# Optimization experiments

Hardware: AMD Instinct MI355X
Metric: run time of the kernel (lower is better)

The kernel has to match this reference:

```python
import jax, jax.numpy as jnp
import numpy as np
from jax import lax

CURRICULUM_EP = 12
LI, LS, LW = 0.5, 0.8, 3.0


def _gauss_win(ws, C, dtype):
    coords = jnp.arange(ws, dtype=jnp.float32) - ws // 2
    g = jnp.exp(-coords ** 2 / (2 * 1.5 ** 2))
    win = g[None, :] * g[:, None]
    win = win / win.sum()
    # depthwise kernel, OIHW with I=1, O=C
    return jnp.broadcast_to(win[None, None], (C, 1, ws, ws)).astype(dtype)


def _dwconv(x, win, p, C):
    return lax.conv_general_dilated(
        x, win, window_strides=(1, 1), padding=[(p, p), (p, p)],
        dimension_numbers=('NCHW', 'OIHW', 'NCHW'), feature_group_count=C)


def diff_ssim(x, y, ws=11):
    C1, C2 = 0.01 ** 2, 0.03 ** 2
    C = x.shape[1]
    p = ws // 2
    win = _gauss_win(ws, C, x.dtype)
    mx = _dwconv(x, win, p, C)
    my = _dwconv(y, win, p, C)
    sxx = _dwconv(x * x, win, p, C) - mx ** 2
    syy = _dwconv(y * y, win, p, C) - my ** 2
    sxy = _dwconv(x * y, win, p, C) - mx * my
    ssim_map = (2 * mx * my + C1) * (2 * sxy + C2) / ((mx ** 2 + my ** 2 + C1) * (sxx + syy + C2))
    return ssim_map.mean()


def setup_inputs() -> dict:
    key = jax.random.key(0)
    k1, k2, k3, k4 = jax.random.split(key, 4)
    B, C, H, W = 16, 3, 512, 512
    NB = 1024  # watermark bits
    eps = 1e-4
    cover = jax.random.uniform(k1, (B, C, H, W), dtype=jnp.float32)
    wmed = jax.random.uniform(k2, (B, C, H, W), dtype=jnp.float32)
    wm_orig = jax.random.uniform(k3, (B, NB), dtype=jnp.float32)
    wm_ext = jnp.clip(jax.random.uniform(k4, (B, NB), dtype=jnp.float32), eps, 1.0 - eps)
    return {"cover": cover, "wmed": wmed, "wm_orig": wm_orig, "wm_ext": wm_ext, "epoch": 20}


def reference(cover, wmed, wm_orig, wm_ext, epoch):
    ml = jnp.mean((wmed - cover) ** 2)
    sv = diff_ssim(wmed, cover)
    sl = 1.0 - sv
    wl = jnp.mean(-(wm_orig * jnp.log(wm_ext) + (1.0 - wm_orig) * jnp.log(1.0 - wm_ext)))
    if epoch <= CURRICULUM_EP:
        w_img, w_ssim = 0.05, 0.05
    else:
        progress = min(1.0, (epoch - CURRICULUM_EP) / 10.0)
        w_img = 0.05 + (LI - 0.05) * progress
        w_ssim = 0.05 + (LS - 0.05) * progress
    total = w_img * ml + w_ssim * sl + LW * wl
    return (total, ml, sv, wl)
```

## Files before the change

### kernel.cpp

```cpp
#include <hip/hip_runtime.h>
#include <math.h>

#define H_IMG 512
#define W_IMG 512
#define TW 32
#define CH 32
#define NCHUNK 4
#define STRIP (CH*NCHUNK)
#define HALO 5
#define WS11 11
#define RING 42
#define RS 36
#define FSTR (RING*RS)
#define NTHREADS 256

typedef float f2 __attribute__((ext_vector_type(2)));

__host__ __device__ constexpr float WT(int t) {
    return (t==0||t==10) ? 0.00102838f :
           (t==1||t==9)  ? 0.00759873f :
           (t==2||t==8)  ? 0.03600075f :
           (t==3||t==7)  ? 0.10936070f :
           (t==4||t==6)  ? 0.21300556f :
           (t==5)        ? 0.26601172f : 0.0f;
}

static __device__ __forceinline__ f2 splat2(float v) { f2 r = {v, v}; return r; }

__global__ __launch_bounds__(NTHREADS, 5) void ssim_mse_tile(
        const float* __restrict__ cover, const float* __restrict__ wmed,
        float* __restrict__ part, int nParts) {
    __shared__ __align__(16) float rbuf[5*FSTR];

    const int tid = threadIdx.x;
    const int bx  = blockIdx.x & 15;
    const int ys  = (blockIdx.x >> 4) & 3;
    const int pl  = blockIdx.x >> 6;
    const size_t pbase = (size_t)pl * (H_IMG*W_IMG);
    const float* xp = wmed + pbase;
    const float* yp = cover + pbase;
    const int Y0  = ys << 7;
    const int tx0 = bx*TW - HALO;
    const bool xin = (bx != 0) && (bx != 15);

    float ssim_acc = 0.f, mse_acc = 0.f;

    for (int k = 0; k < NCHUNK; ++k) {
        const int nrows = (k == 0) ? (CH + 2*HALO) : CH;
        const int hr0   = (k == 0) ? -HALO : (CH*k + HALO);
        const int ntask = nrows << 3;

        for (int t = tid; t < ntask; t += NTHREADS) {
            const int r  = t >> 3, c0 = (t & 7) << 2;
            const int hr = hr0 + r;
            const int gy = Y0 + hr;
            const int slot = (hr + HALO) % RING;
            const bool rok = (unsigned)gy < (unsigned)H_IMG;
            float xv[14], yv[14];
            if (rok && xin) {
                const int ga = tx0 + c0 - 3;
                const float* rx = xp + (size_t)gy*W_IMG + ga;
                const float* ry = yp + (size_t)gy*W_IMG + ga;
                float4 XA = *(const float4*)(rx);
                float4 XB = *(const float4*)(rx + 4);
                float4 XC = *(const float4*)(rx + 8);
                float4 XD = *(const float4*)(rx + 12);
                float  XE = rx[16];
                float4 YA = *(const float4*)(ry);
                float4 YB = *(const float4*)(ry + 4);
                float4 YC = *(const float4*)(ry + 8);
                float4 YD = *(const float4*)(ry + 12);
                float  YE = ry[16];
                xv[0]=XA.w;  xv[1]=XB.x;  xv[2]=XB.y;  xv[3]=XB.z;  xv[4]=XB.w;
                xv[5]=XC.x;  xv[6]=XC.y;  xv[7]=XC.z;  xv[8]=XC.w;  xv[9]=XD.x;
                xv[10]=XD.y; xv[11]=XD.z; xv[12]=XD.w; xv[13]=XE;
                yv[0]=YA.w;  yv[1]=YB.x;  yv[2]=YB.y;  yv[3]=YB.z;  yv[4]=YB.w;
                yv[5]=YC.x;  yv[6]=YC.y;  yv[7]=YC.z;  yv[8]=YC.w;  yv[9]=YD.x;
                yv[10]=YD.y; yv[11]=YD.z; yv[12]=YD.w; yv[13]=YE;
            } else if (rok) {
                const int gc = tx0 + c0;
                const float* prx = xp + (size_t)gy*W_IMG + gc;
                const float* pry = yp + (size_t)gy*W_IMG + gc;
#pragma unroll
                for (int j = 0; j < 14; ++j) {
                    bool ok = (unsigned)(gc + j) < (unsigned)W_IMG;
                    xv[j] = ok ? prx[j] : 0.f;
                    yv[j] = ok ? pry[j] : 0.f;
                }
            } else {
#pragma unroll
                for (int j = 0; j < 14; ++j) { xv[j] = 0.f; yv[j] = 0.f; }
            }

            if ((unsigned)hr < (unsigned)STRIP) {
#pragma unroll
                for (int j = 5; j < 9; ++j) {
                    float d = xv[j] - yv[j];
                    mse_acc = fmaf(d, d, mse_acc);
                }
            }

            f2 A[5][2];
#pragma unroll
            for (int f = 0; f < 5; ++f) { A[f][0] = splat2(0.f); A[f][1] = splat2(0.f); }
#pragma unroll
            for (int j = 0; j < 14; ++j) {
                float px = xv[j], py = yv[j];
                float pxx = px*px, pyy = py*py, pxy = px*py;
#pragma unroll
                for (int p = 0; p < 2; ++p) {
                    const int t0 = j - 2*p;
                    if (t0 >= 0 && t0 <= WS11) {
                        const f2 wp = {WT(t0), WT(t0-1)};
                        A[0][p] = __builtin_elementwise_fma(wp, splat2(px),  A[0][p]);
                        A[1][p] = __builtin_elementwise_fma(wp, splat2(py),  A[1][p]);
                        A[2][p] = __builtin_elementwise_fma(wp, splat2(pxx), A[2][p]);
                        A[3][p] = __builtin_elementwise_fma(wp, splat2(pyy), A[3][p]);
                        A[4][p] = __builtin_elementwise_fma(wp, splat2(pxy), A[4][p]);
                    }
                }
            }
            float* wb = &rbuf[slot*RS + c0];
#pragma unroll
            for (int f = 0; f < 5; ++f) {
                *(float4*)(wb + f*FSTR) =
                    make_float4(A[f][0].x, A[f][0].y, A[f][1].x, A[f][1].y);
            }
        }
        __syncthreads();

        {
            const int c  = tid & 31;
            const int rg = tid >> 3 >> 2;
            const int sb = (CH*k + (rg << 2)) % RING;
            f2 acc[5][2];
#pragma unroll
            for (int f = 0; f < 5; ++f) {
                acc[f][0] = splat2(0.f); acc[f][1] = splat2(0.f);
            }
            const float* bp = rbuf + c;
#pragma unroll
            for (int i = 0; i < 14; ++i) {
                int sl = sb + i; if (sl >= RING) sl -= RING;
                const float* rp = bp + sl*RS;
#pragma unroll
                for (int f = 0; f < 5; ++f) {
                    float v = rp[f*FSTR];
#pragma unroll
                    for (int p = 0; p < 2; ++p) {
                        const int t0 = i - 2*p;
                        if (t0 >= 0 && t0 <= WS11) {
                            const f2 wp = {WT(t0), WT(t0-1)};
                            acc[f][p] = __builtin_elementwise_fma(wp, splat2(v), acc[f][p]);
                        }
                    }
                }
            }
            const f2 c1v = {1e-4f, 1e-4f};
            const f2 c2v = {9e-4f, 9e-4f};
            const f2 two = {2.f, 2.f};
#pragma unroll
            for (int p = 0; p < 2; ++p) {
                f2 mx = acc[0][p], my = acc[1][p];
                f2 sxx = acc[2][p] - mx*mx;
                f2 syy = acc[3][p] - my*my;
                f2 sxy = acc[4][p] - mx*my;
                f2 num = (two*mx*my + c1v) * (two*sxy + c2v);
                f2 den = (mx*mx + my*my + c1v) * (sxx + syy + c2v);
                ssim_acc += __fdividef(num.x, den.x) + __fdividef(num.y, den.y);
            }
        }
        __syncthreads();
    }

#pragma unroll
    for (int off = 32; off > 0; off >>= 1) {
        ssim_acc += __shfl_down(ssim_acc, off);
        mse_acc  += __shfl_down(mse_acc, off);
    }
    const int wid = tid >> 6, lane = tid & 63;
    if (lane == 0) { rbuf[wid] = ssim_acc; rbuf[4+wid] = mse_acc; }
    __syncthreads();
    if (tid == 0) {
        part[blockIdx.x] = rbuf[0]+rbuf[1]+rbuf[2]+rbuf[3];
        part[nParts + blockIdx.x] = rbuf[4]+rbuf[5]+rbuf[6]+rbuf[7];
    }
}

#define FT 1024
__global__ __launch_bounds__(FT) void finalize_k(
        const float* __restrict__ part, int nParts,
        const float* __restrict__ wm_orig, const float* __restrict__ wm_ext,
        int nWm, const int* __restrict__ epoch_p,
        float* __restrict__ out, double inv_npix, double inv_nwm) {
    __shared__ double red[48];
    int tid = threadIdx.x;
    double s_ssim = 0.0, s_mse = 0.0, s_wl = 0.0;
    const float4* s4 = (const float4*)part;
    const float4* m4 = (const float4*)(part + nParts);
    int n4 = nParts >> 2;
    for (int i = tid; i < n4; i += FT) {
        float4 v = s4[i];
        s_ssim += (double)((v.x + v.y) + (v.z + v.w));
        float4 u = m4[i];
        s_mse  += (double)((u.x + u.y) + (u.z + u.w));
    }
    const float4* p4 = (const float4*)wm_orig;
    const float4* q4 = (const float4*)wm_ext;
    int w4 = nWm >> 2;
    for (int i = tid; i < w4; i += FT) {
        float4 p = p4[i], q = q4[i];
        float a;
        a  = -(p.x*__logf(q.x) + (1.f-p.x)*__logf(1.f-q.x));
        a += -(p.y*__logf(q.y) + (1.f-p.y)*__logf(1.f-q.y));
        a += -(p.z*__logf(q.z) + (1.f-p.z)*__logf(1.f-q.z));
        a += -(p.w*__logf(q.w) + (1.f-p.w)*__logf(1.f-q.w));
        s_wl += (double)a;
    }
#pragma unroll
    for (int off = 32; off > 0; off >>= 1) {
        s_ssim += __shfl_down(s_ssim, off);
        s_mse  += __shfl_down(s_mse, off);
        s_wl   += __shfl_down(s_wl, off);
    }
    int wid = tid >> 6, lane = tid & 63;
    if (lane == 0) { red[wid] = s_ssim; red[16+wid] = s_mse; red[32+wid] = s_wl; }
    __syncthreads();
    if (tid == 0) {
        double ssim_sum = 0.0, mse_sum = 0.0, wl_sum = 0.0;
        for (int i = 0; i < 16; ++i) {
            ssim_sum += red[i]; mse_sum += red[16+i]; wl_sum += red[32+i];
        }
        float sv = (float)(ssim_sum * inv_npix);
        float ml = (float)(mse_sum  * inv_npix);
        float wl = (float)(wl_sum   * inv_nwm);
        int e = *epoch_p;
        float w_img, w_ssim;
        if (e <= 12) {
            w_img = 0.05f; w_ssim = 0.05f;
        } else {
            float progress = fminf(1.0f, (float)(e - 12) / 10.0f);
            w_img  = 0.05f + (0.5f - 0.05f)*progress;
            w_ssim = 0.05f + (0.8f - 0.05f)*progress;
        }
        float sl = 1.0f - sv;
        float total = w_img*ml + w_ssim*sl + 3.0f*wl;
        out[0] = total;
        out[1] = ml;
        out[2] = sv;
        out[3] = wl;
    }
}

extern "C" void kernel_launch(void* const* d_in, const int* in_sizes, int n_in,
                              void* d_out, int out_size, void* d_ws, size_t ws_size,
                              hipStream_t stream) {
    const float* cover   = (const float*)d_in[0];
    const float* wmed    = (const float*)d_in[1];
    const float* wm_orig = (const float*)d_in[2];
    const float* wm_ext  = (const float*)d_in[3];
    const int*   epoch   = (const int*)d_in[4];
    float* out = (float*)d_out;

    int npix   = in_sizes[0];
    int planes = npix / (H_IMG * W_IMG);
    int nWm    = in_sizes[2];

    int nBlocks = 16 * 4 * planes;
    int nParts  = nBlocks;
    float* part = (float*)d_ws;

    ssim_mse_tile<<<nBlocks, NTHREADS, 0, stream>>>(cover, wmed, part, nParts);
    finalize_k<<<1, FT, 0, stream>>>(part, nParts, wm_orig, wm_ext, nWm,
                                     epoch, out,
                                     1.0 / (double)npix, 1.0 / (double)nWm);
}
```

Before: 176.6 us.

## Filter sum/difference moments to cut SSIM convolved fields from five to four

Rewrites the SSIM statistics in terms of s=x+y and d=x-y, so only four fields (s, d, s², d²) are convolved instead of five (x, y, x², y², xy). The SSIM numerator and denominator terms are then recovered algebraically from these moments. This cuts horizontal and vertical FMAs and LDS traffic by about a fifth, and the smaller shared buffer allows raising the occupancy hint from 5 to 6 blocks per CU. In exchange, the cancellation when forming products from differences of squared terms can slightly change floating-point accuracy.

```diff
diff --git a/kernel.cpp b/kernel.cpp
--- a/kernel.cpp
+++ b/kernel.cpp
@@ -12,6 +12,7 @@
 #define RING 42
 #define RS 36
 #define FSTR (RING*RS)
+#define NF 4
 #define NTHREADS 256
 
 typedef float f2 __attribute__((ext_vector_type(2)));
@@ -27,10 +28,10 @@
 
 static __device__ __forceinline__ f2 splat2(float v) { f2 r = {v, v}; return r; }
 
-__global__ __launch_bounds__(NTHREADS, 5) void ssim_mse_tile(
+__global__ __launch_bounds__(NTHREADS, 6) void ssim_mse_tile(
         const float* __restrict__ cover, const float* __restrict__ wmed,
         float* __restrict__ part, int nParts) {
-    __shared__ __align__(16) float rbuf[5*FSTR];
+    __shared__ __align__(16) float rbuf[NF*FSTR];
 
     const int tid = threadIdx.x;
     const int bx  = blockIdx.x & 15;
@@ -92,37 +93,34 @@
                 for (int j = 0; j < 14; ++j) { xv[j] = 0.f; yv[j] = 0.f; }
             }
 
-            if ((unsigned)hr < (unsigned)STRIP) {
-#pragma unroll
-                for (int j = 5; j < 9; ++j) {
-                    float d = xv[j] - yv[j];
-                    mse_acc = fmaf(d, d, mse_acc);
-                }
-            }
-
-            f2 A[5][2];
-#pragma unroll
-            for (int f = 0; f < 5; ++f) { A[f][0] = splat2(0.f); A[f][1] = splat2(0.f); }
+            const bool own = (unsigned)hr < (unsigned)STRIP;
+
+            f2 A[NF][2];
+#pragma unroll
+            for (int f = 0; f < NF; ++f) { A[f][0] = splat2(0.f); A[f][1] = splat2(0.f); }
 #pragma unroll
             for (int j = 0; j < 14; ++j) {
-                float px = xv[j], py = yv[j];
-                float pxx = px*px, pyy = py*py, pxy = px*py;
+                float sj = xv[j] + yv[j];
+                float dj = xv[j] - yv[j];
+                float s2 = sj*sj, d2 = dj*dj;
+                if (j >= 5 && j < 9) {
+                    if (own) mse_acc += d2;
+                }
 #pragma unroll
                 for (int p = 0; p < 2; ++p) {
                     const int t0 = j - 2*p;
                     if (t0 >= 0 && t0 <= WS11) {
                         const f2 wp = {WT(t0), WT(t0-1)};
-                        A[0][p] = __builtin_elementwise_fma(wp, splat2(px),  A[0][p]);
-                        A[1][p] = __builtin_elementwise_fma(wp, splat2(py),  A[1][p]);
-                        A[2][p] = __builtin_elementwise_fma(wp, splat2(pxx), A[2][p]);
-                        A[3][p] = __builtin_elementwise_fma(wp, splat2(pyy), A[3][p]);
-                        A[4][p] = __builtin_elementwise_fma(wp, splat2(pxy), A[4][p]);
+                        A[0][p] = __builtin_elementwise_fma(wp, splat2(sj), A[0][p]);
+                        A[1][p] = __builtin_elementwise_fma(wp, splat2(dj), A[1][p]);
+                        A[2][p] = __builtin_elementwise_fma(wp, splat2(s2), A[2][p]);
+                        A[3][p] = __builtin_elementwise_fma(wp, splat2(d2), A[3][p]);
                     }
                 }
             }
             float* wb = &rbuf[slot*RS + c0];
 #pragma unroll
-            for (int f = 0; f < 5; ++f) {
+            for (int f = 0; f < NF; ++f) {
                 *(float4*)(wb + f*FSTR) =
                     make_float4(A[f][0].x, A[f][0].y, A[f][1].x, A[f][1].y);
             }
@@ -131,11 +129,11 @@
 
         {
             const int c  = tid & 31;
-            const int rg = tid >> 3 >> 2;
+            const int rg = tid >> 5;
             const int sb = (CH*k + (rg << 2)) % RING;
-            f2 acc[5][2];
-#pragma unroll
-            for (int f = 0; f < 5; ++f) {
+            f2 acc[NF][2];
+#pragma unroll
+            for (int f = 0; f < NF; ++f) {
                 acc[f][0] = splat2(0.f); acc[f][1] = splat2(0.f);
             }
             const float* bp = rbuf + c;
@@ -144,7 +142,7 @@
                 int sl = sb + i; if (sl >= RING) sl -= RING;
                 const float* rp = bp + sl*RS;
 #pragma unroll
-                for (int f = 0; f < 5; ++f) {
+                for (int f = 0; f < NF; ++f) {
                     float v = rp[f*FSTR];
 #pragma unroll
                     for (int p = 0; p < 2; ++p) {
@@ -158,15 +156,18 @@
             }
             const f2 c1v = {1e-4f, 1e-4f};
             const f2 c2v = {9e-4f, 9e-4f};
-            const f2 two = {2.f, 2.f};
+            const f2 half = {0.5f, 0.5f};
 #pragma unroll
             for (int p = 0; p < 2; ++p) {
-                f2 mx = acc[0][p], my = acc[1][p];
-                f2 sxx = acc[2][p] - mx*mx;
-                f2 syy = acc[3][p] - my*my;
-                f2 sxy = acc[4][p] - mx*my;
-                f2 num = (two*mx*my + c1v) * (two*sxy + c2v);
-                f2 den = (mx*mx + my*my + c1v) * (sxx + syy + c2v);
+                f2 S = acc[0][p], D = acc[1][p];
+                f2 Cs = acc[2][p], Cd = acc[3][p];
+                f2 SS = S*S, DD = D*D;
+                f2 mxmy2 = (SS - DD) * half;
+                f2 msq   = (SS + DD) * half;
+                f2 sxy2  = (Cs - Cd) * half - mxmy2;
+                f2 ssum  = (Cs + Cd) * half - msq;
+                f2 num = (mxmy2 + c1v) * (sxy2 + c2v);
+                f2 den = (msq + c1v) * (ssum + c2v);
                 ssim_acc += __fdividef(num.x, den.x) + __fdividef(num.y, den.y);
             }
         }
```

Measured after the change: 174.7 us. Within noise of the previous version (-1.1%).
